# Kernel tuning notes

Hardware: AMD Instinct MI355X
Metric: run time of the kernel (lower is better)

Reference implementation:

```python
import jax, jax.numpy as jnp
import numpy as np

EPS = 1e-12  # torch F.normalize eps


def _l2norm(v, axis):
    n = jnp.sqrt(jnp.sum(v * v, axis=axis, keepdims=True))
    return v / jnp.maximum(n, EPS)


def setup_inputs() -> dict:
    key = jax.random.key(0)
    k1, k2, k3 = jax.random.split(key, 3)
    N, D, H, W, K = 64, 256, 64, 64, 64
    x = jax.random.normal(k1, (N, D, H, W), dtype=jnp.float32)
    conv_weight = jax.random.normal(k2, (K, D), dtype=jnp.float32)
    centroids = jax.random.uniform(k3, (K, D), dtype=jnp.float32)
    return {"x": x, "conv_weight": conv_weight, "centroids": centroids}


def reference(x, conv_weight, centroids):
    # x: [N, D, H, W]; conv_weight: [K, D] (1x1 conv); centroids: [K, D]
    N, D, H, W = x.shape
    K = centroids.shape[0]
    x = _l2norm(x, axis=1)                       # descriptor-wise L2 norm over D
    xf = x.reshape(N, D, H * W)                  # [N, D, L]
    # 1x1 conv == matmul over channel dim: [N, K, L]
    logits = jnp.einsum('kd,ndl->nkl', conv_weight, xf)
    a = jax.nn.softmax(logits, axis=1)           # softmax over clusters
    # vlad[n,k,d] = sum_l a[n,k,l] * (x[n,d,l] - c[k,d])
    #            = (a @ x^T)[n,k,d] - (sum_l a[n,k,l]) * c[k,d]
    vlad = jnp.einsum('nkl,ndl->nkd', a, xf) - a.sum(axis=2)[:, :, None] * centroids[None]
    vlad = _l2norm(vlad, axis=2)                 # intra-normalization
    vlad = vlad.reshape(N, K * D)
    vlad = _l2norm(vlad, axis=1)                 # global L2 norm
    return vlad
```

## Files before the change

kernel.cpp:

```cpp
#include <hip/hip_runtime.h>

typedef unsigned short u16;
typedef short bf16x8 __attribute__((ext_vector_type(8)));
typedef float f32x4  __attribute__((ext_vector_type(4)));

#define NN 64
#define DD 256
#define LL 4096
#define KK 64
#define CHUNK 1024
#define LS 64
#define NSUB 16

__device__ __forceinline__ u16 f2bf(float f) {
  union { float f; unsigned int i; } v; v.f = f;
  unsigned int u = v.i;
  return (u16)((u + 0x7FFFu + ((u >> 16) & 1u)) >> 16);
}
__device__ __forceinline__ float bf2f(u16 u) {
  union { unsigned int i; float f; } v; v.i = ((unsigned int)u) << 16; return v.f;
}

__global__ void zero_ws_kernel(float* __restrict__ p, int n4) {
  int i = blockIdx.x * 256 + threadIdx.x;
  if (i < n4) ((f32x4*)p)[i] = (f32x4){0.f, 0.f, 0.f, 0.f};
}

__global__ __launch_bounds__(256, 1) void netvlad_main(
    const float* __restrict__ xg, const float* __restrict__ wg,
    float* __restrict__ Sg, float* __restrict__ Ag) {
  __shared__ u16  x_dl[DD * LS];
  __shared__ u16  x_ld[LS * DD];
  __shared__ float lg[LS * KK];
  __shared__ u16  akl[KK * LS];
  __shared__ float pn[32 * LS];
  __shared__ float rno[LS];

  const int tid  = threadIdx.x;
  const int w    = tid >> 6;
  const int lane = tid & 63;
  const int quad = lane >> 4;
  const int l15  = lane & 15;
  const int dblk = tid >> 3;
  const int lblk = tid & 7;
  const int n    = blockIdx.x >> 2;
  const int ch   = blockIdx.x & 3;

  bf16x8 aw[8];
  {
    const float* wp = wg + (w * 16 + l15) * DD + quad * 8;
#pragma unroll
    for (int s = 0; s < 8; ++s) {
      f32x4 wa = *(const f32x4*)(wp + s * 32);
      f32x4 wb = *(const f32x4*)(wp + s * 32 + 4);
      bf16x8 t;
#pragma unroll
      for (int j = 0; j < 4; ++j) { t[j] = (short)f2bf(wa[j]); t[j + 4] = (short)f2bf(wb[j]); }
      aw[s] = t;
    }
  }

  f32x4 acc2[16];
#pragma unroll
  for (int i = 0; i < 16; ++i) acc2[i] = (f32x4){0.f, 0.f, 0.f, 0.f};
  float regA = 0.f;

  const float* xbase = xg + (size_t)n * DD * LL + (size_t)ch * CHUNK;

  f32x4 ga[8], gb[8];
#pragma unroll
  for (int r = 0; r < 8; ++r) {
    const float* p = xbase + (size_t)(dblk * 8 + r) * LL + lblk * 8;
    ga[r] = *(const f32x4*)p;
    gb[r] = *(const f32x4*)(p + 4);
  }

  for (int it = 0; it < NSUB; ++it) {
    float pj[8];
#pragma unroll
    for (int j = 0; j < 8; ++j) pj[j] = 0.f;
#pragma unroll
    for (int r = 0; r < 8; ++r)
#pragma unroll
      for (int j = 0; j < 4; ++j) {
        pj[j]     += ga[r][j] * ga[r][j];
        pj[j + 4] += gb[r][j] * gb[r][j];
      }
    *(f32x4*)&pn[dblk * 64 + lblk * 8]     = (f32x4){pj[0], pj[1], pj[2], pj[3]};
    *(f32x4*)&pn[dblk * 64 + lblk * 8 + 4] = (f32x4){pj[4], pj[5], pj[6], pj[7]};
    __syncthreads();
    if (tid < 64) {
      float s = 0.f;
#pragma unroll
      for (int db = 0; db < 32; ++db) s += pn[db * 64 + tid];
      rno[tid] = 1.f / fmaxf(sqrtf(s), 1e-12f);
    }
    __syncthreads();

    float rn[8];
#pragma unroll
    for (int j = 0; j < 8; ++j) rn[j] = rno[lblk * 8 + j];
    u16 xn[8][8];
#pragma unroll
    for (int r = 0; r < 8; ++r)
#pragma unroll
      for (int j = 0; j < 4; ++j) {
        xn[r][j]     = f2bf(ga[r][j] * rn[j]);
        xn[r][j + 4] = f2bf(gb[r][j] * rn[j + 4]);
      }
#pragma unroll
    for (int r = 0; r < 8; ++r) {
      bf16x8 row;
#pragma unroll
      for (int j = 0; j < 8; ++j) row[j] = (short)xn[r][j];
      *(bf16x8*)&x_dl[(dblk * 8 + r) * 64 + ((lblk ^ r) * 8)] = row;
    }
#pragma unroll
    for (int j = 0; j < 8; ++j) {
      bf16x8 col;
#pragma unroll
      for (int r = 0; r < 8; ++r) col[r] = (short)xn[r][j];
      int lam = lblk * 8 + j;
      *(bf16x8*)&x_ld[lam * 256 + ((dblk ^ (lam & 31)) * 8)] = col;
    }

    if (it + 1 < NSUB) {
      const float* p = xbase + (it + 1) * LS;
#pragma unroll
      for (int r = 0; r < 8; ++r) {
        const float* q = p + (size_t)(dblk * 8 + r) * LL + lblk * 8;
        ga[r] = *(const f32x4*)q;
        gb[r] = *(const f32x4*)(q + 4);
      }
    }
    __syncthreads();

    f32x4 acc1[4];
#pragma unroll
    for (int lt = 0; lt < 4; ++lt) acc1[lt] = (f32x4){0.f, 0.f, 0.f, 0.f};
#pragma unroll
    for (int s = 0; s < 8; ++s) {
#pragma unroll
      for (int lt = 0; lt < 4; ++lt) {
        int lam = lt * 16 + l15;
        bf16x8 b = *(const bf16x8*)&x_ld[lam * 256 + (((s * 4 + quad) ^ (lam & 31)) * 8)];
        acc1[lt] = __builtin_amdgcn_mfma_f32_16x16x32_bf16(aw[s], b, acc1[lt], 0, 0, 0);
      }
    }
#pragma unroll
    for (int lt = 0; lt < 4; ++lt) {
      int lam = lt * 16 + l15;
      *(f32x4*)&lg[lam * 64 + (((w * 4 + quad) ^ (lam & 15)) * 4)] = acc1[lt];
    }
    __syncthreads();

    if (tid < 64) {
      const int lam = tid, sw = lam & 15;
      float mx = -1e30f;
#pragma unroll
      for (int c = 0; c < 16; ++c) {
        f32x4 v = *(const f32x4*)&lg[lam * 64 + ((c ^ sw) * 4)];
        mx = fmaxf(mx, fmaxf(fmaxf(v[0], v[1]), fmaxf(v[2], v[3])));
      }
      float sum = 0.f;
#pragma unroll
      for (int c = 0; c < 16; ++c) {
        f32x4 v = *(const f32x4*)&lg[lam * 64 + ((c ^ sw) * 4)];
#pragma unroll
        for (int i = 0; i < 4; ++i) sum += __expf(v[i] - mx);
      }
      float rs = 1.f / sum;
#pragma unroll
      for (int c = 0; c < 16; ++c) {
        f32x4 v = *(const f32x4*)&lg[lam * 64 + ((c ^ sw) * 4)];
#pragma unroll
        for (int i = 0; i < 4; ++i) {
          int k = c * 4 + i;
          float a = __expf(v[i] - mx) * rs;
          akl[k * 64 + (((lam >> 3) ^ (k & 7)) * 8) + (lam & 7)] = f2bf(a);
        }
      }
    }
    __syncthreads();

#pragma unroll
    for (int s = 0; s < 2; ++s) {
      int kk = w * 16 + l15;
      bf16x8 aA = *(const bf16x8*)&akl[kk * 64 + (((s * 4 + quad) ^ (kk & 7)) * 8)];
#pragma unroll
      for (int dt = 0; dt < 16; ++dt) {
        int d = dt * 16 + l15;
        bf16x8 bX = *(const bf16x8*)&x_dl[d * 64 + (((s * 4 + quad) ^ (d & 7)) * 8)];
        acc2[dt] = __builtin_amdgcn_mfma_f32_16x16x32_bf16(aA, bX, acc2[dt], 0, 0, 0);
      }
    }
    if (tid < 64) {
      const int k = tid;
#pragma unroll
      for (int c = 0; c < 8; ++c) {
        bf16x8 v = *(const bf16x8*)&akl[k * 64 + ((c ^ (k & 7)) * 8)];
#pragma unroll
        for (int j = 0; j < 8; ++j) regA += bf2f((u16)v[j]);
      }
    }
    __syncthreads();
  }

  float* Sn = Sg + ((size_t)n * KK * DD);
#pragma unroll
  for (int dt = 0; dt < 16; ++dt) {
#pragma unroll
    for (int r = 0; r < 4; ++r) {
      int k = w * 16 + quad * 4 + r;
      int d = dt * 16 + l15;
      atomicAdd(&Sn[k * DD + d], acc2[dt][r]);
    }
  }
  if (tid < 64) atomicAdd(&Ag[n * KK + tid], regA);
}

__global__ __launch_bounds__(256, 1) void netvlad_fin(
    const float* __restrict__ Sg, const float* __restrict__ Ag,
    const float* __restrict__ cg, float* __restrict__ outg) {
  __shared__ float red[256];
  __shared__ float tot[64];
  __shared__ float rk[64];
  __shared__ float gsh;
  const int n = blockIdx.x, tid = threadIdx.x;
  const int k = tid >> 2, part = tid & 3;
  const float* Sp = Sg + ((size_t)n * KK + k) * DD + part * 64;
  const float* cp = cg + k * DD + part * 64;
  const float Ak  = Ag[n * KK + k];
  float v[64];
  float s2 = 0.f;
#pragma unroll
  for (int j = 0; j < 64; ++j) {
    float t = Sp[j] - Ak * cp[j];
    v[j] = t;
    s2 += t * t;
  }
  red[tid] = s2;
  __syncthreads();
  if (tid < 64) {
    float s = red[tid * 4] + red[tid * 4 + 1] + red[tid * 4 + 2] + red[tid * 4 + 3];
    float r = 1.f / fmaxf(sqrtf(s), 1e-12f);
    rk[tid]  = r;
    tot[tid] = s * r * r;
  }
  __syncthreads();
  if (tid == 0) {
    float t = 0.f;
    for (int i = 0; i < 64; ++i) t += tot[i];
    gsh = 1.f / fmaxf(sqrtf(t), 1e-12f);
  }
  __syncthreads();
  const float sc = rk[k] * gsh;
  float* op = outg + ((size_t)n * KK + k) * DD + part * 64;
#pragma unroll
  for (int j0 = 0; j0 < 64; j0 += 4) {
    f32x4 o;
#pragma unroll
    for (int jj = 0; jj < 4; ++jj) o[jj] = v[j0 + jj] * sc;
    *(f32x4*)(op + j0) = o;
  }
}

extern "C" void kernel_launch(void* const* d_in, const int* in_sizes, int n_in,
                              void* d_out, int out_size, void* d_ws, size_t ws_size,
                              hipStream_t stream) {
  const float* x   = (const float*)d_in[0];
  const float* wgt = (const float*)d_in[1];
  const float* cen = (const float*)d_in[2];
  float* out = (float*)d_out;

  float* S = (float*)d_ws;
  float* A = S + (size_t)NN * KK * DD;

  const int n4 = (NN * KK * DD + NN * KK) / 4;
  hipLaunchKernelGGL(zero_ws_kernel, dim3((n4 + 255) / 256), dim3(256), 0, stream, S, n4);
  hipLaunchKernelGGL(netvlad_main, dim3(NN * 4), dim3(256), 0, stream, x, wgt, S, A);
  hipLaunchKernelGGL(netvlad_fin, dim3(NN), dim3(256), 0, stream, S, A, cen, out);
}
```

Before: 428.6 us.

## Restructure NetVLAD: fold norm into logits, register softmax, per-block partials

Splits each sample across 8 chunks instead of 4 and raises the launch bound to 2 blocks per CU. The per-descriptor L2 norm becomes shuffle reductions and is applied by scaling the logits and assignments, so x goes to bf16 unnormalized. Softmax is computed in registers from the MFMA accumulators with a cross-wave shared sum, dropping the logits buffer and several barriers. Softmax runs without max subtraction, and bf16 rounding is simplified to round-half-up. When workspace allows, blocks write partial S/A slices without atomics and the finalize kernel reduces them, which skips the zeroing kernel but adds extra global traffic.

New measurement: 498.3 us. 16.3% more time.

```diff
diff --git a/kernel.cpp b/kernel.cpp
--- a/kernel.cpp
+++ b/kernel.cpp
@@ -8,17 +8,15 @@
 #define DD 256
 #define LL 4096
 #define KK 64
-#define CHUNK 1024
+#define CHUNK 512
 #define LS 64
-#define NSUB 16
+#define NSUB 8
+#define NCH 8
+#define SSZ (KK*DD)
 
 __device__ __forceinline__ u16 f2bf(float f) {
   union { float f; unsigned int i; } v; v.f = f;
-  unsigned int u = v.i;
-  return (u16)((u + 0x7FFFu + ((u >> 16) & 1u)) >> 16);
-}
-__device__ __forceinline__ float bf2f(u16 u) {
-  union { unsigned int i; float f; } v; v.i = ((unsigned int)u) << 16; return v.f;
+  return (u16)((v.i + 0x8000u) >> 16);
 }
 
 __global__ void zero_ws_kernel(float* __restrict__ p, int n4) {
@@ -26,15 +24,15 @@
   if (i < n4) ((f32x4*)p)[i] = (f32x4){0.f, 0.f, 0.f, 0.f};
 }
 
-__global__ __launch_bounds__(256, 1) void netvlad_main(
+template <bool PARTIAL>
+__global__ __launch_bounds__(256, 2) void netvlad_main(
     const float* __restrict__ xg, const float* __restrict__ wg,
     float* __restrict__ Sg, float* __restrict__ Ag) {
   __shared__ u16  x_dl[DD * LS];
   __shared__ u16  x_ld[LS * DD];
-  __shared__ float lg[LS * KK];
   __shared__ u16  akl[KK * LS];
-  __shared__ float pn[32 * LS];
-  __shared__ float rno[LS];
+  __shared__ float pnw[4 * LS];
+  __shared__ float wsum[4 * LS];
 
   const int tid  = threadIdx.x;
   const int w    = tid >> 6;
@@ -43,8 +41,9 @@
   const int l15  = lane & 15;
   const int dblk = tid >> 3;
   const int lblk = tid & 7;
-  const int n    = blockIdx.x >> 2;
-  const int ch   = blockIdx.x & 3;
+  const int dw   = lane >> 3;
+  const int n    = blockIdx.x >> 3;
+  const int ch   = blockIdx.x & 7;
 
   bf16x8 aw[8];
   {
@@ -63,9 +62,9 @@
   f32x4 acc2[16];
 #pragma unroll
   for (int i = 0; i < 16; ++i) acc2[i] = (f32x4){0.f, 0.f, 0.f, 0.f};
-  float regA = 0.f;
-
-  const float* xbase = xg + (size_t)n * DD * LL + (size_t)ch * CHUNK;
+  float regAk[4] = {0.f, 0.f, 0.f, 0.f};
+
+  const float* xbase = xg + (size_t)n * DD * LL + ch * CHUNK;
 
   f32x4 ga[8], gb[8];
 #pragma unroll
@@ -86,27 +85,22 @@
         pj[j]     += ga[r][j] * ga[r][j];
         pj[j + 4] += gb[r][j] * gb[r][j];
       }
-    *(f32x4*)&pn[dblk * 64 + lblk * 8]     = (f32x4){pj[0], pj[1], pj[2], pj[3]};
-    *(f32x4*)&pn[dblk * 64 + lblk * 8 + 4] = (f32x4){pj[4], pj[5], pj[6], pj[7]};
-    __syncthreads();
-    if (tid < 64) {
-      float s = 0.f;
-#pragma unroll
-      for (int db = 0; db < 32; ++db) s += pn[db * 64 + tid];
-      rno[tid] = 1.f / fmaxf(sqrtf(s), 1e-12f);
-    }
-    __syncthreads();
-
-    float rn[8];
-#pragma unroll
-    for (int j = 0; j < 8; ++j) rn[j] = rno[lblk * 8 + j];
+#pragma unroll
+    for (int o = 8; o <= 32; o <<= 1)
+#pragma unroll
+      for (int j = 0; j < 8; ++j) pj[j] += __shfl_xor(pj[j], o);
+    if (dw == 0) {
+      *(f32x4*)&pnw[w * 64 + lblk * 8]     = (f32x4){pj[0], pj[1], pj[2], pj[3]};
+      *(f32x4*)&pnw[w * 64 + lblk * 8 + 4] = (f32x4){pj[4], pj[5], pj[6], pj[7]};
+    }
+
     u16 xn[8][8];
 #pragma unroll
     for (int r = 0; r < 8; ++r)
 #pragma unroll
       for (int j = 0; j < 4; ++j) {
-        xn[r][j]     = f2bf(ga[r][j] * rn[j]);
-        xn[r][j + 4] = f2bf(gb[r][j] * rn[j + 4]);
+        xn[r][j]     = f2bf(ga[r][j]);
+        xn[r][j + 4] = f2bf(gb[r][j]);
       }
 #pragma unroll
     for (int r = 0; r < 8; ++r) {
@@ -147,38 +141,34 @@
         acc1[lt] = __builtin_amdgcn_mfma_f32_16x16x32_bf16(aw[s], b, acc1[lt], 0, 0, 0);
       }
     }
+    float rno[4], e[4][4], psum[4];
 #pragma unroll
     for (int lt = 0; lt < 4; ++lt) {
-      int lam = lt * 16 + l15;
-      *(f32x4*)&lg[lam * 64 + (((w * 4 + quad) ^ (lam & 15)) * 4)] = acc1[lt];
-    }
-    __syncthreads();
-
-    if (tid < 64) {
-      const int lam = tid, sw = lam & 15;
-      float mx = -1e30f;
-#pragma unroll
-      for (int c = 0; c < 16; ++c) {
-        f32x4 v = *(const f32x4*)&lg[lam * 64 + ((c ^ sw) * 4)];
-        mx = fmaxf(mx, fmaxf(fmaxf(v[0], v[1]), fmaxf(v[2], v[3])));
-      }
-      float sum = 0.f;
-#pragma unroll
-      for (int c = 0; c < 16; ++c) {
-        f32x4 v = *(const f32x4*)&lg[lam * 64 + ((c ^ sw) * 4)];
-#pragma unroll
-        for (int i = 0; i < 4; ++i) sum += __expf(v[i] - mx);
-      }
-      float rs = 1.f / sum;
-#pragma unroll
-      for (int c = 0; c < 16; ++c) {
-        f32x4 v = *(const f32x4*)&lg[lam * 64 + ((c ^ sw) * 4)];
-#pragma unroll
-        for (int i = 0; i < 4; ++i) {
-          int k = c * 4 + i;
-          float a = __expf(v[i] - mx) * rs;
-          akl[k * 64 + (((lam >> 3) ^ (k & 7)) * 8) + (lam & 7)] = f2bf(a);
-        }
+      int l = lt * 16 + l15;
+      float s = pnw[l] + pnw[64 + l] + pnw[128 + l] + pnw[192 + l];
+      rno[lt] = rsqrtf(fmaxf(s, 1e-24f));
+      float ps = 0.f;
+#pragma unroll
+      for (int r = 0; r < 4; ++r) { e[lt][r] = __expf(acc1[lt][r] * rno[lt]); ps += e[lt][r]; }
+      ps += __shfl_xor(ps, 16);
+      ps += __shfl_xor(ps, 32);
+      psum[lt] = ps;
+    }
+    float pw = quad == 0 ? psum[0] : quad == 1 ? psum[1] : quad == 2 ? psum[2] : psum[3];
+    wsum[w * 64 + quad * 16 + l15] = pw;
+    __syncthreads();
+
+#pragma unroll
+    for (int lt = 0; lt < 4; ++lt) {
+      int l = lt * 16 + l15;
+      float rs = 1.f / (wsum[l] + wsum[64 + l] + wsum[128 + l] + wsum[192 + l]);
+      float rr = rs * rno[lt];
+#pragma unroll
+      for (int r = 0; r < 4; ++r) {
+        float sm = e[lt][r] * rs;
+        regAk[r] += sm;
+        int k = w * 16 + quad * 4 + r;
+        akl[k * 64 + (((l >> 3) ^ (k & 7)) * 8) + (l & 7)] = f2bf(e[lt][r] * rr);
       }
     }
     __syncthreads();
@@ -194,74 +184,81 @@
         acc2[dt] = __builtin_amdgcn_mfma_f32_16x16x32_bf16(aA, bX, acc2[dt], 0, 0, 0);
       }
     }
-    if (tid < 64) {
-      const int k = tid;
-#pragma unroll
-      for (int c = 0; c < 8; ++c) {
-        bf16x8 v = *(const bf16x8*)&akl[k * 64 + ((c ^ (k & 7)) * 8)];
-#pragma unroll
-        for (int j = 0; j < 8; ++j) regA += bf2f((u16)v[j]);
-      }
-    }
-    __syncthreads();
-  }
-
-  float* Sn = Sg + ((size_t)n * KK * DD);
-#pragma unroll
-  for (int dt = 0; dt < 16; ++dt) {
-#pragma unroll
-    for (int r = 0; r < 4; ++r) {
-      int k = w * 16 + quad * 4 + r;
-      int d = dt * 16 + l15;
-      atomicAdd(&Sn[k * DD + d], acc2[dt][r]);
-    }
-  }
-  if (tid < 64) atomicAdd(&Ag[n * KK + tid], regA);
-}
-
-__global__ __launch_bounds__(256, 1) void netvlad_fin(
+    __syncthreads();
+  }
+
+  if (PARTIAL) {
+    float* Sp = Sg + (size_t)blockIdx.x * SSZ;
+#pragma unroll
+    for (int dt = 0; dt < 16; ++dt)
+#pragma unroll
+      for (int r = 0; r < 4; ++r)
+        Sp[(w * 16 + quad * 4 + r) * DD + dt * 16 + l15] = acc2[dt][r];
+  } else {
+    float* Sn = Sg + (size_t)n * SSZ;
+#pragma unroll
+    for (int dt = 0; dt < 16; ++dt)
+#pragma unroll
+      for (int r = 0; r < 4; ++r)
+        atomicAdd(&Sn[(w * 16 + quad * 4 + r) * DD + dt * 16 + l15], acc2[dt][r]);
+  }
+#pragma unroll
+  for (int o = 1; o <= 8; o <<= 1)
+#pragma unroll
+    for (int r = 0; r < 4; ++r) regAk[r] += __shfl_xor(regAk[r], o);
+  if (l15 == 0) {
+    if (PARTIAL) {
+      float* Ap = Ag + (size_t)blockIdx.x * KK;
+#pragma unroll
+      for (int r = 0; r < 4; ++r) Ap[w * 16 + quad * 4 + r] = regAk[r];
+    } else {
+#pragma unroll
+      for (int r = 0; r < 4; ++r) atomicAdd(&Ag[n * KK + w * 16 + quad * 4 + r], regAk[r]);
+    }
+  }
+}
+
+__global__ __launch_bounds__(256, 2) void netvlad_fin(
     const float* __restrict__ Sg, const float* __restrict__ Ag,
-    const float* __restrict__ cg, float* __restrict__ outg) {
-  __shared__ float red[256];
-  __shared__ float tot[64];
-  __shared__ float rk[64];
-  __shared__ float gsh;
+    const float* __restrict__ cg, float* __restrict__ outg, int nsl) {
+  __shared__ float wtot[4];
   const int n = blockIdx.x, tid = threadIdx.x;
-  const int k = tid >> 2, part = tid & 3;
-  const float* Sp = Sg + ((size_t)n * KK + k) * DD + part * 64;
-  const float* cp = cg + k * DD + part * 64;
-  const float Ak  = Ag[n * KK + k];
-  float v[64];
-  float s2 = 0.f;
-#pragma unroll
-  for (int j = 0; j < 64; ++j) {
-    float t = Sp[j] - Ak * cp[j];
-    v[j] = t;
-    s2 += t * t;
-  }
-  red[tid] = s2;
+  const int w = tid >> 6, lane = tid & 63;
+  const float* Sb = Sg + (size_t)n * nsl * SSZ;
+  const float* Ab = Ag + (size_t)n * nsl * KK;
+
+  f32x4 v[16];
+  float rk[16];
+  float tot = 0.f;
+#pragma unroll
+  for (int i = 0; i < 16; ++i) {
+    const int k = w * 16 + i;
+    float Ak = 0.f;
+    for (int sl = 0; sl < nsl; ++sl) Ak += Ab[sl * KK + k];
+    f32x4 s = (f32x4){0.f, 0.f, 0.f, 0.f};
+    for (int sl = 0; sl < nsl; ++sl)
+      s += *(const f32x4*)&Sb[(size_t)sl * SSZ + k * DD + lane * 4];
+    f32x4 c4 = *(const f32x4*)&cg[k * DD + lane * 4];
+    f32x4 t = s - Ak * c4;
+    v[i] = t;
+    float q = t[0] * t[0] + t[1] * t[1] + t[2] * t[2] + t[3] * t[3];
+#pragma unroll
+    for (int o = 1; o <= 32; o <<= 1) q += __shfl_xor(q, o);
+    float r = 1.f / fmaxf(sqrtf(q), 1e-12f);
+    rk[i] = r;
+    tot += q * r * r;
+  }
+  if (lane == 0) wtot[w] = tot;
   __syncthreads();
-  if (tid < 64) {
-    float s = red[tid * 4] + red[tid * 4 + 1] + red[tid * 4 + 2] + red[tid * 4 + 3];
-    float r = 1.f / fmaxf(sqrtf(s), 1e-12f);
-    rk[tid]  = r;
-    tot[tid] = s * r * r;
-  }
-  __syncthreads();
-  if (tid == 0) {
-    float t = 0.f;
-    for (int i = 0; i < 64; ++i) t += tot[i];
-    gsh = 1.f / fmaxf(sqrtf(t), 1e-12f);
-  }
-  __syncthreads();
-  const float sc = rk[k] * gsh;
-  float* op = outg + ((size_t)n * KK + k) * DD + part * 64;
-#pragma unroll
-  for (int j0 = 0; j0 < 64; j0 += 4) {
-    f32x4 o;
-#pragma unroll
-    for (int jj = 0; jj < 4; ++jj) o[jj] = v[j0 + jj] * sc;
-    *(f32x4*)(op + j0) = o;
+  const float g = wtot[0] + wtot[1] + wtot[2] + wtot[3];
+  const float gs = 1.f / fmaxf(sqrtf(g), 1e-12f);
+#pragma unroll
+  for (int i = 0; i < 16; ++i) {
+    const int k = w * 16 + i;
+    const float sc = rk[i] * gs;
+    f32x4 o = v[i];
+    o[0] *= sc; o[1] *= sc; o[2] *= sc; o[3] *= sc;
+    *(f32x4*)&outg[(size_t)n * SSZ + k * DD + lane * 4] = o;
   }
 }
 
@@ -273,11 +270,19 @@
   const float* cen = (const float*)d_in[2];
   float* out = (float*)d_out;
 
-  float* S = (float*)d_ws;
-  float* A = S + (size_t)NN * KK * DD;
-
-  const int n4 = (NN * KK * DD + NN * KK) / 4;
-  hipLaunchKernelGGL(zero_ws_kernel, dim3((n4 + 255) / 256), dim3(256), 0, stream, S, n4);
-  hipLaunchKernelGGL(netvlad_main, dim3(NN * 4), dim3(256), 0, stream, x, wgt, S, A);
-  hipLaunchKernelGGL(netvlad_fin, dim3(NN), dim3(256), 0, stream, S, A, cen, out);
-}
+  const size_t nblk = (size_t)NN * NCH;
+  const size_t need = nblk * SSZ * 4 + nblk * KK * 4;
+  if (ws_size >= need) {
+    float* Sp = (float*)d_ws;
+    float* Ap = Sp + nblk * SSZ;
+    hipLaunchKernelGGL((netvlad_main<true>), dim3(NN * NCH), dim3(256), 0, stream, x, wgt, Sp, Ap);
+    hipLaunchKernelGGL(netvlad_fin, dim3(NN), dim3(256), 0, stream, Sp, Ap, cen, out, NCH);
+  } else {
+    float* S = (float*)d_ws;
+    float* A = S + (size_t)NN * SSZ;
+    const int n4 = (NN * SSZ + NN * KK) / 4;
+    hipLaunchKernelGGL(zero_ws_kernel, dim3((n4 + 255) / 256), dim3(256), 0, stream, S, n4);
+    hipLaunchKernelGGL((netvlad_main<false>), dim3(NN * NCH), dim3(256), 0, stream, x, wgt, S, A);
+    hipLaunchKernelGGL(netvlad_fin, dim3(NN), dim3(256), 0, stream, S, A, cen, out, 1);
+  }
+}
```
